# Optimization experiments

Hardware: AMD Instinct MI355X
Metric: run time of the kernel (lower is better)

## Reference

```python
import jax, jax.numpy as jnp
import numpy as np

B, T, C, H = 8, 2048, 1024, 64

def setup_inputs() -> dict:
    key = jax.random.key(0)
    k1, k2, k3, k4 = jax.random.split(key, 4)
    x = jax.random.normal(k1, (B, T, C), dtype=jnp.float32)
    # torch nn.Linear default init ~ U(-1/sqrt(in), 1/sqrt(in)); scale kept small for stability
    s = 1.0 / np.sqrt(C)
    Wq = jax.random.uniform(k2, (C, H), dtype=jnp.float32, minval=-s, maxval=s)
    Wk = jax.random.uniform(k3, (C, H), dtype=jnp.float32, minval=-s, maxval=s)
    Wv = jax.random.uniform(k4, (C, H), dtype=jnp.float32, minval=-s, maxval=s)
    return {"x": x, "Wq": Wq, "Wk": Wk, "Wv": Wv}

def reference(x, Wq, Wk, Wv):
    # x: [B,T,C]; Wq/Wk/Wv: [C,H] (equivalent to torch Linear weight transposed)
    Q = jnp.einsum('btc,ch->bth', x, Wq)
    K = jnp.einsum('btc,ch->bth', x, Wk)
    V = jnp.einsum('btc,ch->bth', x, Wv)
    H_ = Q.shape[-1]
    scale = 1.0 / jnp.sqrt(jnp.asarray(H_, dtype=Q.dtype))
    w = jnp.einsum('bqh,bkh->bqk', Q, K) * scale  # [B,T,T]
    T_ = x.shape[1]
    causal = jnp.tril(jnp.ones((T_, T_), dtype=bool))
    w = jnp.where(causal, w, -jnp.inf)
    w = jax.nn.softmax(w, axis=-1)
    out = jnp.einsum('bqk,bkh->bqh', w, V)  # [B,T,H]
    return out
```

## Files before the change

### kernel.cpp

```cpp
#include <hip/hip_runtime.h>
#include <math.h>

#define Bb 8
#define Tt 2048
#define Cc 1024
#define Hh 64
#define BT (Bb * Tt)
#define SLOG2E 0.18033688011112042f

typedef __attribute__((ext_vector_type(8))) short short8;
typedef __attribute__((ext_vector_type(4))) short s16x4;
typedef __attribute__((ext_vector_type(4))) float floatx4;
typedef __attribute__((ext_vector_type(4))) unsigned int uint4v;

__device__ inline unsigned short f2bf(float f) {
  unsigned int u = __builtin_bit_cast(unsigned int, f);
  u += 0x7fff + ((u >> 16) & 1);
  return (unsigned short)(u >> 16);
}
__device__ inline float bf2f(unsigned short u) {
  unsigned int x = ((unsigned int)u) << 16;
  return __builtin_bit_cast(float, x);
}

__device__ inline short8 cvt8(const float4& u, const float4& v) {
  unsigned int p0, p1, p2, p3;
  asm("v_cvt_pk_bf16_f32 %0, %1, %2" : "=v"(p0) : "v"(u.x), "v"(u.y));
  asm("v_cvt_pk_bf16_f32 %0, %1, %2" : "=v"(p1) : "v"(u.z), "v"(u.w));
  asm("v_cvt_pk_bf16_f32 %0, %1, %2" : "=v"(p2) : "v"(v.x), "v"(v.y));
  asm("v_cvt_pk_bf16_f32 %0, %1, %2" : "=v"(p3) : "v"(v.z), "v"(v.w));
  uint4v w; w[0] = p0; w[1] = p1; w[2] = p2; w[3] = p3;
  return __builtin_bit_cast(short8, w);
}

__global__ __launch_bounds__(256) void wconv2(
    const float* __restrict__ Wq, const float* __restrict__ Wk,
    const float* __restrict__ Wv, unsigned short* __restrict__ WTf) {
  int bid = blockIdx.x;
  int w = bid >> 5;
  int kc = bid & 31;
  const float* __restrict__ W = (w == 0) ? Wq : (w == 1 ? Wk : Wv);
  int t = threadIdx.x;
  int hg = t >> 6, quad = (t >> 4) & 3, lrow = t & 15;
  int g = w * 4 + hg;
  int h = hg * 16 + lrow;
  unsigned short tmp[8];
#pragma unroll
  for (int j = 0; j < 8; ++j)
    tmp[j] = f2bf(W[(size_t)(kc * 32 + quad * 8 + j) * Hh + h]);
  unsigned short* dst = &WTf[((size_t)(g * 32 + kc) * 64 + quad * 16 + lrow) * 8];
  *(ushort4*)dst = make_ushort4(tmp[0], tmp[1], tmp[2], tmp[3]);
  *(ushort4*)(dst + 4) = make_ushort4(tmp[4], tmp[5], tmp[6], tmp[7]);
}

__global__ __launch_bounds__(256) void qkv6(
    const float* __restrict__ x, const unsigned short* __restrict__ WTf,
    unsigned short* __restrict__ Qb, unsigned short* __restrict__ Kb,
    unsigned short* __restrict__ VTt) {
  int mt = blockIdx.x;
  int t = threadIdx.x;
  int wv = t >> 6, lane = t & 63;
  int lrow = lane & 15, quad = lane >> 4;

  floatx4 acc[2][3];
#pragma unroll
  for (int g2 = 0; g2 < 2; ++g2)
#pragma unroll
    for (int j = 0; j < 3; ++j)
#pragma unroll
      for (int r = 0; r < 4; ++r) acc[g2][j][r] = 0.f;

  const unsigned short* wbase[3];
#pragma unroll
  for (int j = 0; j < 3; ++j)
    wbase[j] = WTf + (size_t)(wv * 3 + j) * 32 * 512 + lane * 8;

  const float* xrow[2];
#pragma unroll
  for (int g2 = 0; g2 < 2; ++g2)
    xrow[g2] = x + (size_t)(mt * 32 + g2 * 16 + lrow) * Cc + quad * 8;

#pragma unroll 4
  for (int kk = 0; kk < 16; ++kk) {
    short8 af[2][2];
#pragma unroll
    for (int g2 = 0; g2 < 2; ++g2)
#pragma unroll
      for (int kc2 = 0; kc2 < 2; ++kc2) {
        float4 u = *(const float4*)(xrow[g2] + kk * 64 + kc2 * 32);
        float4 v = *(const float4*)(xrow[g2] + kk * 64 + kc2 * 32 + 4);
        af[g2][kc2] = cvt8(u, v);
      }
    short8 bf[3][2];
    int kg = kk * 2;
#pragma unroll
    for (int j = 0; j < 3; ++j)
#pragma unroll
      for (int kc2 = 0; kc2 < 2; ++kc2)
        bf[j][kc2] = *(const short8*)(wbase[j] + (size_t)(kg + kc2) * 512);
#pragma unroll
    for (int g2 = 0; g2 < 2; ++g2)
#pragma unroll
      for (int j = 0; j < 3; ++j) {
        acc[g2][j] = __builtin_amdgcn_mfma_f32_16x16x32_bf16(af[g2][0], bf[j][0], acc[g2][j], 0, 0, 0);
        acc[g2][j] = __builtin_amdgcn_mfma_f32_16x16x32_bf16(af[g2][1], bf[j][1], acc[g2][j], 0, 0, 0);
      }
  }

#pragma unroll
  for (int g2 = 0; g2 < 2; ++g2) {
    int tok0 = mt * 32 + g2 * 16 + quad * 4;
#pragma unroll
    for (int j = 0; j < 3; ++j) {
      int nbase = (wv * 3 + j) * 16;
      if (nbase >= 128) {
        int h = nbase - 128 + lrow;
        *(ushort4*)&VTt[(size_t)(tok0 >> 6) * 4096 + h * 64 + (tok0 & 63)] =
            make_ushort4(f2bf(acc[g2][j][0]), f2bf(acc[g2][j][1]),
                         f2bf(acc[g2][j][2]), f2bf(acc[g2][j][3]));
      } else {
        unsigned short* dst = (nbase >= 64) ? Kb : Qb;
        float sc = (nbase >= 64) ? 1.0f : SLOG2E;
        int col = (nbase & 63) + lrow;
#pragma unroll
        for (int r = 0; r < 4; ++r)
          dst[(size_t)(tok0 + r) * Hh + col] = f2bf(acc[g2][j][r] * sc);
      }
    }
  }
}

__global__ __launch_bounds__(512) void attn3(
    const unsigned short* __restrict__ Qb, const unsigned short* __restrict__ Kb,
    const unsigned short* __restrict__ VTt, float* __restrict__ out) {
  __shared__ __align__(16) unsigned char smem[33 * 1024];
  unsigned short* Pall = (unsigned short*)smem;
  unsigned short* Ocomb = (unsigned short*)smem;
  float* Lcomb = (float*)(smem + 32768);

  int bid = blockIdx.x;
  int b = bid >> 5;
  int j = bid & 31;
  int t = threadIdx.x;
  int wv = t >> 6, lane = t & 63;
  int lrow = lane & 15, quad = lane >> 4;

  unsigned short* Pw = Pall + wv * 2048;
  unsigned int pbase = (unsigned int)(size_t)Pw;

  unsigned int paddr[2][2];
#pragma unroll
  for (int qs = 0; qs < 2; ++qs)
#pragma unroll
    for (int kc = 0; kc < 2; ++kc)
      paddr[qs][kc] = pbase + (unsigned int)(qs * 2048 + kc * 1024 + quad * 256 + lrow * 8);

  int wbase_off = (lrow >> 2) * 64 + (lrow & 3) * 16 + quad * 4;

  short8 ones;
#pragma unroll
  for (int i = 0; i < 8; ++i) ones[i] = (short)0x3F80;

  for (int half = 0; half < 2; ++half) {
    int qt = half ? (63 - j) : j;
    int q0 = qt * 32;
    int nkt = (qt >> 1) + 1;

    short8 aq[2][2];
#pragma unroll
    for (int qs = 0; qs < 2; ++qs)
#pragma unroll
      for (int kc = 0; kc < 2; ++kc)
        aq[qs][kc] = *(const short8*)
            &Qb[(size_t)(b * Tt + q0 + qs * 16 + lrow) * Hh + kc * 32 + quad * 8];

    floatx4 acc_o[2][4];
    floatx4 acc_l[2];
#pragma unroll
    for (int qs = 0; qs < 2; ++qs) {
#pragma unroll
      for (int r = 0; r < 4; ++r) acc_l[qs][r] = 0.f;
#pragma unroll
      for (int hs = 0; hs < 4; ++hs)
#pragma unroll
        for (int r = 0; r < 4; ++r) acc_o[qs][hs][r] = 0.f;
    }

    for (int kt = wv; kt < nkt; kt += 8) {
      int kbase = b * Tt + kt * 64;
      short8 kf[4][2], vf[4][2];
#pragma unroll
      for (int sn = 0; sn < 4; ++sn)
#pragma unroll
        for (int kc = 0; kc < 2; ++kc)
          kf[sn][kc] = *(const short8*)
              &Kb[(size_t)(kbase + sn * 16 + lrow) * Hh + kc * 32 + quad * 8];
      int ktile = b * 32 + kt;
#pragma unroll
      for (int hs = 0; hs < 4; ++hs)
#pragma unroll
        for (int kc = 0; kc < 2; ++kc)
          vf[hs][kc] = *(const short8*)
              &VTt[(size_t)ktile * 4096 + (hs * 16 + lrow) * 64 + kc * 32 + quad * 8];

      floatx4 s[2][4];
      __builtin_amdgcn_s_setprio(1);
#pragma unroll
      for (int qs = 0; qs < 2; ++qs)
#pragma unroll
        for (int sn = 0; sn < 4; ++sn) {
          floatx4 z;
#pragma unroll
          for (int r = 0; r < 4; ++r) z[r] = 0.f;
          z = __builtin_amdgcn_mfma_f32_16x16x32_bf16(aq[qs][0], kf[sn][0], z, 0, 0, 0);
          z = __builtin_amdgcn_mfma_f32_16x16x32_bf16(aq[qs][1], kf[sn][1], z, 0, 0, 0);
          s[qs][sn] = z;
        }
      __builtin_amdgcn_s_setprio(0);

      bool diag = (kt == nkt - 1);
#pragma unroll
      for (int qs = 0; qs < 2; ++qs)
#pragma unroll
        for (int sn = 0; sn < 4; ++sn) {
          float p[4];
#pragma unroll
          for (int r = 0; r < 4; ++r) {
            float v = s[qs][sn][r];
            if (diag) {
              int gk = kt * 64 + sn * 16 + lrow;
              int gq = q0 + qs * 16 + quad * 4 + r;
              if (gk > gq) v = -INFINITY;
            }
            p[r] = __builtin_amdgcn_exp2f(v);
          }
          unsigned int w0, w1;
          asm("v_cvt_pk_bf16_f32 %0, %1, %2" : "=v"(w0) : "v"(p[0]), "v"(p[1]));
          asm("v_cvt_pk_bf16_f32 %0, %1, %2" : "=v"(w1) : "v"(p[2]), "v"(p[3]));
          int woff = qs * 1024 + (sn >> 1) * 512 + (sn & 1) * 256 + wbase_off;
          *(uint2*)&Pw[woff] = make_uint2(w0, w1);
        }

      asm volatile("s_waitcnt lgkmcnt(0)" ::: "memory");
      short8 ap[2][2];
#pragma unroll
      for (int qs = 0; qs < 2; ++qs)
#pragma unroll
        for (int kc = 0; kc < 2; ++kc) {
          s16x4 lo, hi;
          asm volatile("ds_read_b64_tr_b16 %0, %1"
                       : "=v"(lo) : "v"(paddr[qs][kc]) : "memory");
          asm volatile("ds_read_b64_tr_b16 %0, %1 offset:128"
                       : "=v"(hi) : "v"(paddr[qs][kc]) : "memory");
          ap[qs][kc] = __builtin_shufflevector(lo, hi, 0, 1, 2, 3, 4, 5, 6, 7);
        }
      asm volatile("s_waitcnt lgkmcnt(0)" ::: "memory");
      __builtin_amdgcn_sched_barrier(0);

      __builtin_amdgcn_s_setprio(1);
#pragma unroll
      for (int qs = 0; qs < 2; ++qs) {
        acc_l[qs] = __builtin_amdgcn_mfma_f32_16x16x32_bf16(ap[qs][0], ones, acc_l[qs], 0, 0, 0);
        acc_l[qs] = __builtin_amdgcn_mfma_f32_16x16x32_bf16(ap[qs][1], ones, acc_l[qs], 0, 0, 0);
#pragma unroll
        for (int hs = 0; hs < 4; ++hs) {
          acc_o[qs][hs] = __builtin_amdgcn_mfma_f32_16x16x32_bf16(ap[qs][0], vf[hs][0], acc_o[qs][hs], 0, 0, 0);
          acc_o[qs][hs] = __builtin_amdgcn_mfma_f32_16x16x32_bf16(ap[qs][1], vf[hs][1], acc_o[qs][hs], 0, 0, 0);
        }
      }
      __builtin_amdgcn_s_setprio(0);
    }

#pragma unroll
    for (int qs = 0; qs < 2; ++qs)
#pragma unroll
      for (int hs = 0; hs < 4; ++hs) {
        int s8 = qs * 4 + hs;
        *(ushort4*)&Ocomb[((wv * 8 + s8) * 64 + lane) * 4] =
            make_ushort4(f2bf(acc_o[qs][hs][0]), f2bf(acc_o[qs][hs][1]),
                         f2bf(acc_o[qs][hs][2]), f2bf(acc_o[qs][hs][3]));
      }
    if (lrow == 0) {
#pragma unroll
      for (int qs = 0; qs < 2; ++qs)
#pragma unroll
        for (int r = 0; r < 4; ++r)
          Lcomb[wv * 32 + qs * 16 + quad * 4 + r] = acc_l[qs][r];
    }
    __syncthreads();

    {
      int qsub = wv >> 2, hs = wv & 3;
      float o[4] = {0.f, 0.f, 0.f, 0.f};
#pragma unroll
      for (int w = 0; w < 8; ++w) {
        ushort4 pk = *(const ushort4*)&Ocomb[((w * 8 + wv) * 64 + lane) * 4];
        o[0] += bf2f(pk.x); o[1] += bf2f(pk.y);
        o[2] += bf2f(pk.z); o[3] += bf2f(pk.w);
      }
#pragma unroll
      for (int r = 0; r < 4; ++r) {
        float lv = 0.f;
#pragma unroll
        for (int w = 0; w < 8; ++w)
          lv += Lcomb[w * 32 + qsub * 16 + quad * 4 + r];
        int row = q0 + qsub * 16 + quad * 4 + r;
        out[(size_t)(b * Tt + row) * Hh + hs * 16 + lrow] = o[r] / lv;
      }
    }
    __syncthreads();
  }
}

extern "C" void kernel_launch(void* const* d_in, const int* in_sizes, int n_in,
                              void* d_out, int out_size, void* d_ws, size_t ws_size,
                              hipStream_t stream) {
  const float* x = (const float*)d_in[0];
  const float* Wq = (const float*)d_in[1];
  const float* Wk = (const float*)d_in[2];
  const float* Wv = (const float*)d_in[3];
  float* out = (float*)d_out;

  unsigned short* WTf = (unsigned short*)d_ws;
  unsigned short* Qb = WTf + 192 * 1024;
  unsigned short* Kb = Qb + (size_t)BT * Hh;
  unsigned short* VTt = Kb + (size_t)BT * Hh;

  wconv2<<<dim3(96), dim3(256), 0, stream>>>(Wq, Wk, Wv, WTf);
  qkv6<<<dim3(512), dim3(256), 0, stream>>>(x, WTf, Qb, Kb, VTt);
  attn3<<<dim3(256), dim3(512), 0, stream>>>(Qb, Kb, VTt, out);
}
```

Before: 161.0 us.

## Stage x tiles into swizzled LDS via async global_load_lds triple buffering

The QKV projection kernel now loads each 32x64 fp32 tile of x into a triple-buffered shared-memory ring using direct global-to-LDS loads, one step ahead of compute, instead of having each lane read x straight from global memory. An XOR swizzle on the column index is meant to avoid LDS bank conflicts when lanes read their MFMA fragments. The aim is to overlap x fetches with MFMA work and make the global reads coalesced. In exchange it adds a __syncthreads per k-step and 24 KB of LDS per block, which may reduce occupancy.

```diff
diff --git a/kernel.cpp b/kernel.cpp
--- a/kernel.cpp
+++ b/kernel.cpp
@@ -53,10 +53,12 @@
   *(ushort4*)(dst + 4) = make_ushort4(tmp[4], tmp[5], tmp[6], tmp[7]);
 }
 
-__global__ __launch_bounds__(256) void qkv6(
+__global__ __launch_bounds__(256) void qkv9(
     const float* __restrict__ x, const unsigned short* __restrict__ WTf,
     unsigned short* __restrict__ Qb, unsigned short* __restrict__ Kb,
     unsigned short* __restrict__ VTt) {
+  __shared__ __align__(16) float xs[3 * 2048];
+
   int mt = blockIdx.x;
   int t = threadIdx.x;
   int wv = t >> 6, lane = t & 63;
@@ -75,20 +77,49 @@
   for (int j = 0; j < 3; ++j)
     wbase[j] = WTf + (size_t)(wv * 3 + j) * 32 * 512 + lane * 8;
 
-  const float* xrow[2];
+  int r0 = t >> 4, c0 = t & 15;
+  int cs0 = c0 ^ (((r0 & 7) << 1) | ((r0 >> 3) & 1));
+  const float* gsrc0 = x + ((size_t)(mt * 32) + r0) * Cc + cs0 * 4;
+  const float* gsrc1 = x + ((size_t)(mt * 32) + r0 + 16) * Cc + cs0 * 4;
+
+  int msk = ((lrow & 7) << 1) | ((lrow >> 3) & 1);
+  int roff[2][2][2];
 #pragma unroll
   for (int g2 = 0; g2 < 2; ++g2)
-    xrow[g2] = x + (size_t)(mt * 32 + g2 * 16 + lrow) * Cc + quad * 8;
-
-#pragma unroll 4
+#pragma unroll
+    for (int kc2 = 0; kc2 < 2; ++kc2)
+#pragma unroll
+      for (int h = 0; h < 2; ++h)
+        roff[g2][kc2][h] = (g2 * 16 + lrow) * 256 +
+                           (((kc2 * 8 + quad * 2 + h) ^ msk) << 4);
+
+  auto stage = [&](int kk) {
+    const float* s0 = gsrc0 + kk * 64;
+    const float* s1 = gsrc1 + kk * 64;
+    char* d0 = (char*)xs + (kk % 3) * 8192 + t * 16;
+    char* d1 = d0 + 4096;
+    __builtin_amdgcn_global_load_lds(
+        (const __attribute__((address_space(1))) void*)s0,
+        (__attribute__((address_space(3))) void*)d0, 16, 0, 0);
+    __builtin_amdgcn_global_load_lds(
+        (const __attribute__((address_space(1))) void*)s1,
+        (__attribute__((address_space(3))) void*)d1, 16, 0, 0);
+  };
+
+  stage(0);
+#pragma unroll
   for (int kk = 0; kk < 16; ++kk) {
+    if (kk + 1 < 16) stage(kk + 1);
+    __syncthreads();
+
+    const char* bufc = (const char*)xs + (kk % 3) * 8192;
     short8 af[2][2];
 #pragma unroll
     for (int g2 = 0; g2 < 2; ++g2)
 #pragma unroll
       for (int kc2 = 0; kc2 < 2; ++kc2) {
-        float4 u = *(const float4*)(xrow[g2] + kk * 64 + kc2 * 32);
-        float4 v = *(const float4*)(xrow[g2] + kk * 64 + kc2 * 32 + 4);
+        float4 u = *(const float4*)(bufc + roff[g2][kc2][0]);
+        float4 v = *(const float4*)(bufc + roff[g2][kc2][1]);
         af[g2][kc2] = cvt8(u, v);
       }
     short8 bf[3][2];
@@ -327,6 +358,6 @@
   unsigned short* VTt = Kb + (size_t)BT * Hh;
 
   wconv2<<<dim3(96), dim3(256), 0, stream>>>(Wq, Wk, Wv, WTf);
-  qkv6<<<dim3(512), dim3(256), 0, stream>>>(x, WTf, Qb, Kb, VTt);
+  qkv9<<<dim3(512), dim3(256), 0, stream>>>(x, WTf, Qb, Kb, VTt);
   attn3<<<dim3(256), dim3(512), 0, stream>>>(Qb, Kb, VTt, out);
 }
```

Measured after the change: 134.8 us. 16.2% less time.

## Stage converted x tile in LDS and halve QKV projection tile rows

Applied to the files above, without the earlier changes.

The QKV projection kernel now processes 16 tokens per block instead of 32, doubling the grid to 1024 blocks. Half of the threads load each x chunk once, convert it to bf16 and write it to a swizzled LDS buffer, prefetching the next chunk into registers. All four waves then read their A fragments from LDS instead of each wave re-reading and re-converting the same x rows from global memory. This removes redundant global loads and conversions and adds parallelism, at the cost of two barriers per k-step and twice as many weight fragment loads across the grid.

```diff
diff --git a/kernel.cpp b/kernel.cpp
--- a/kernel.cpp
+++ b/kernel.cpp
@@ -53,44 +53,57 @@
   *(ushort4*)(dst + 4) = make_ushort4(tmp[4], tmp[5], tmp[6], tmp[7]);
 }
 
-__global__ __launch_bounds__(256) void qkv6(
+__global__ __launch_bounds__(256) void qkv10(
     const float* __restrict__ x, const unsigned short* __restrict__ WTf,
     unsigned short* __restrict__ Qb, unsigned short* __restrict__ Kb,
     unsigned short* __restrict__ VTt) {
+  __shared__ __align__(16) unsigned short Af[1024];
+
   int mt = blockIdx.x;
   int t = threadIdx.x;
   int wv = t >> 6, lane = t & 63;
   int lrow = lane & 15, quad = lane >> 4;
 
-  floatx4 acc[2][3];
-#pragma unroll
-  for (int g2 = 0; g2 < 2; ++g2)
-#pragma unroll
-    for (int j = 0; j < 3; ++j)
-#pragma unroll
-      for (int r = 0; r < 4; ++r) acc[g2][j][r] = 0.f;
+  floatx4 acc[3];
+#pragma unroll
+  for (int j = 0; j < 3; ++j)
+#pragma unroll
+    for (int r = 0; r < 4; ++r) acc[j][r] = 0.f;
+
+  int srow = t >> 3, scg = t & 7;
+  int skc2 = scg >> 2, squad = scg & 3;
+  int sslot = skc2 * 64 + squad * 16 + ((srow + squad + 4 * skc2) & 15);
+  const float* xp = x + (size_t)(mt * 16 + (srow & 15)) * Cc + scg * 8;
+  bool stager = (t < 128);
+
+  int aslot[2];
+#pragma unroll
+  for (int kc2 = 0; kc2 < 2; ++kc2)
+    aslot[kc2] = (kc2 * 64 + quad * 16 + ((lrow + quad + 4 * kc2) & 15)) * 8;
 
   const unsigned short* wbase[3];
 #pragma unroll
   for (int j = 0; j < 3; ++j)
     wbase[j] = WTf + (size_t)(wv * 3 + j) * 32 * 512 + lane * 8;
 
-  const float* xrow[2];
-#pragma unroll
-  for (int g2 = 0; g2 < 2; ++g2)
-    xrow[g2] = x + (size_t)(mt * 32 + g2 * 16 + lrow) * Cc + quad * 8;
-
-#pragma unroll 4
+  float4 nv0, nv1;
+  if (stager) {
+    nv0 = *(const float4*)xp;
+    nv1 = *(const float4*)(xp + 4);
+  }
+
   for (int kk = 0; kk < 16; ++kk) {
-    short8 af[2][2];
-#pragma unroll
-    for (int g2 = 0; g2 < 2; ++g2)
-#pragma unroll
-      for (int kc2 = 0; kc2 < 2; ++kc2) {
-        float4 u = *(const float4*)(xrow[g2] + kk * 64 + kc2 * 32);
-        float4 v = *(const float4*)(xrow[g2] + kk * 64 + kc2 * 32 + 4);
-        af[g2][kc2] = cvt8(u, v);
-      }
+    __syncthreads();
+    if (stager) {
+      short8 a = cvt8(nv0, nv1);
+      *(short8*)&Af[sslot * 8] = a;
+      if (kk < 15) {
+        nv0 = *(const float4*)(xp + (kk + 1) * 64);
+        nv1 = *(const float4*)(xp + (kk + 1) * 64 + 4);
+      }
+    }
+    __syncthreads();
+
     short8 bf[3][2];
     int kg = kk * 2;
 #pragma unroll
@@ -98,33 +111,34 @@
 #pragma unroll
       for (int kc2 = 0; kc2 < 2; ++kc2)
         bf[j][kc2] = *(const short8*)(wbase[j] + (size_t)(kg + kc2) * 512);
-#pragma unroll
-    for (int g2 = 0; g2 < 2; ++g2)
-#pragma unroll
-      for (int j = 0; j < 3; ++j) {
-        acc[g2][j] = __builtin_amdgcn_mfma_f32_16x16x32_bf16(af[g2][0], bf[j][0], acc[g2][j], 0, 0, 0);
-        acc[g2][j] = __builtin_amdgcn_mfma_f32_16x16x32_bf16(af[g2][1], bf[j][1], acc[g2][j], 0, 0, 0);
-      }
+    short8 af[2];
+#pragma unroll
+    for (int kc2 = 0; kc2 < 2; ++kc2)
+      af[kc2] = *(const short8*)&Af[aslot[kc2]];
+#pragma unroll
+    for (int j = 0; j < 3; ++j) {
+      acc[j] = __builtin_amdgcn_mfma_f32_16x16x32_bf16(af[0], bf[j][0], acc[j], 0, 0, 0);
+      acc[j] = __builtin_amdgcn_mfma_f32_16x16x32_bf16(af[1], bf[j][1], acc[j], 0, 0, 0);
+    }
   }
 
-#pragma unroll
-  for (int g2 = 0; g2 < 2; ++g2) {
-    int tok0 = mt * 32 + g2 * 16 + quad * 4;
+  {
+    int tok0 = mt * 16 + quad * 4;
 #pragma unroll
     for (int j = 0; j < 3; ++j) {
       int nbase = (wv * 3 + j) * 16;
       if (nbase >= 128) {
         int h = nbase - 128 + lrow;
         *(ushort4*)&VTt[(size_t)(tok0 >> 6) * 4096 + h * 64 + (tok0 & 63)] =
-            make_ushort4(f2bf(acc[g2][j][0]), f2bf(acc[g2][j][1]),
-                         f2bf(acc[g2][j][2]), f2bf(acc[g2][j][3]));
+            make_ushort4(f2bf(acc[j][0]), f2bf(acc[j][1]),
+                         f2bf(acc[j][2]), f2bf(acc[j][3]));
       } else {
         unsigned short* dst = (nbase >= 64) ? Kb : Qb;
         float sc = (nbase >= 64) ? 1.0f : SLOG2E;
         int col = (nbase & 63) + lrow;
 #pragma unroll
         for (int r = 0; r < 4; ++r)
-          dst[(size_t)(tok0 + r) * Hh + col] = f2bf(acc[g2][j][r] * sc);
+          dst[(size_t)(tok0 + r) * Hh + col] = f2bf(acc[j][r] * sc);
       }
     }
   }
@@ -327,6 +341,6 @@
   unsigned short* VTt = Kb + (size_t)BT * Hh;
 
   wconv2<<<dim3(96), dim3(256), 0, stream>>>(Wq, Wk, Wv, WTf);
-  qkv6<<<dim3(512), dim3(256), 0, stream>>>(x, WTf, Qb, Kb, VTt);
+  qkv10<<<dim3(1024), dim3(256), 0, stream>>>(x, WTf, Qb, Kb, VTt);
   attn3<<<dim3(256), dim3(512), 0, stream>>>(Qb, Kb, VTt, out);
 }
```

After: 139.8 us. -13.1%, faster.
